# Performance work log

Measured on AMD Instinct MI355X. Metric: run time of the kernel, lower is better.

Reference implementation:

```python
import jax, jax.numpy as jnp
import numpy as np

N, E, H, ED = 10000, 160000, 512, 16
EPS = 1e-5
EDGE_SCALE = 0.1

def _ln(x, g, b):
    mu = jnp.mean(x, axis=-1, keepdims=True)
    var = jnp.mean(jnp.square(x - mu), axis=-1, keepdims=True)
    return (x - mu) * jax.lax.rsqrt(var + EPS) * g + b

def setup_inputs() -> dict:
    key = jax.random.key(0)
    ks = jax.random.split(key, 16)
    def w(k, i, o):
        return jax.random.normal(k, (i, o), jnp.float32) * (1.0 / np.sqrt(i))
    return {
        "h": jax.random.normal(ks[0], (N, H), jnp.float32),
        "edge_attr": jax.random.normal(ks[1], (E, ED), jnp.float32),
        "msg_w1": w(ks[2], H + ED, H), "msg_b1": jnp.zeros((H,), jnp.float32),
        "msg_w2": w(ks[3], H, H),      "msg_b2": jnp.zeros((H,), jnp.float32),
        "upd_w1": w(ks[4], 2 * H, H),  "upd_b1": jnp.zeros((H,), jnp.float32),
        "upd_w2": w(ks[5], H, H),      "upd_b2": jnp.zeros((H,), jnp.float32),
        "norm_g": jnp.ones((H,), jnp.float32), "norm_b": jnp.zeros((H,), jnp.float32),
        "em_w1": w(ks[6], 2 * H + ED, ED), "em_b1": jnp.zeros((ED,), jnp.float32),
        "em_w2": w(ks[7], ED, ED),         "em_b2": jnp.zeros((ED,), jnp.float32),
        "eg_w": w(ks[8], 2 * H + ED, 1),   "eg_b": jnp.zeros((1,), jnp.float32),
        "en_g": jnp.ones((ED,), jnp.float32), "en_b": jnp.zeros((ED,), jnp.float32),
        "edge_index": jax.random.randint(ks[9], (2, E), 0, N, jnp.int32),
    }

def reference(h, edge_attr, msg_w1, msg_b1, msg_w2, msg_b2,
              upd_w1, upd_b1, upd_w2, upd_b2, norm_g, norm_b,
              em_w1, em_b1, em_w2, em_b2, eg_w, eg_b, en_g, en_b,
              edge_index):
    src, dst = edge_index[0], edge_index[1]
    hs = h[src]                      # (E, H)
    hd = h[dst]                      # (E, H)
    # edge update with gating + scaled residual (eval: keep mask == 1)
    z = jnp.concatenate([hs, hd, edge_attr], axis=-1)   # (E, 2H+ED)
    gate = jax.nn.sigmoid(z @ eg_w + eg_b)               # (E, 1)
    delta = jax.nn.gelu(z @ em_w1 + em_b1, approximate=False) @ em_w2 + em_b2
    e_new = _ln(edge_attr + EDGE_SCALE * gate * delta, en_g, en_b)
    # message computation + scatter-add aggregation
    zm = jnp.concatenate([hs, e_new], axis=-1)           # (E, H+ED)
    m = jax.nn.gelu(zm @ msg_w1 + msg_b1, approximate=False) @ msg_w2 + msg_b2
    agg = jax.ops.segment_sum(m, dst, num_segments=h.shape[0])  # (N, H)
    # node update + residual + LayerNorm
    zu = jnp.concatenate([h, agg], axis=-1)              # (N, 2H)
    h2 = jax.nn.gelu(zu @ upd_w1 + upd_b1, approximate=False) @ upd_w2 + upd_b2
    h_out = _ln(h + h2, norm_g, norm_b)
    return (h_out, e_new)
```

## Files before the change

kernel.cpp:

```cpp
#include <hip/hip_runtime.h>

#define N_NODES 10000
#define N_EDGES 160000
#define HD 512
#define EDD 16

typedef unsigned short u16;
typedef __attribute__((ext_vector_type(8))) short bf16x8;
typedef __attribute__((ext_vector_type(4))) float f32x4;
typedef unsigned int u32;

__device__ __forceinline__ float bf2f(u16 u){
  unsigned int x = ((unsigned int)u) << 16;
  return __builtin_bit_cast(float, x);
}
__device__ __forceinline__ u16 f2bf(float f){
  unsigned int x = __builtin_bit_cast(unsigned int, f);
  unsigned int r = (x + 0x7fffu + ((x >> 16) & 1u)) >> 16;
  return (u16)r;
}
__device__ __forceinline__ float ldx(const void* p, long long i, int f32){
  return f32 ? ((const float*)p)[i] : bf2f(((const u16*)p)[i]);
}
__device__ __forceinline__ void stx(void* p, long long i, int f32, float v){
  if (f32) ((float*)p)[i] = v; else ((u16*)p)[i] = f2bf(v);
}
__device__ __forceinline__ float gelu_f(float x){
  float c = x * x;
  float a = x * (1.5957691216f + 0.0713548162f * c);
  float e = __expf(-a);
  return x * __builtin_amdgcn_rcpf(1.0f + e);
}
__device__ __forceinline__ f32x4 mfma16(bf16x8 a, bf16x8 b, f32x4 c){
  return __builtin_amdgcn_mfma_f32_16x16x32_bf16(a, b, c, 0, 0, 0);
}
__device__ __forceinline__ int swz8(int row, int slot){
  return (slot ^ ((row >> 1) & 3)) * 8;
}
__device__ __forceinline__ bf16x8 ld8(const void* p, long long i, int f32){
  if (!f32) return *(const bf16x8*)((const u16*)p + i);
  const float* q = (const float*)p + i;
  float4 a = *(const float4*)q, b = *(const float4*)(q + 4);
  u16 t[8] = { f2bf(a.x), f2bf(a.y), f2bf(a.z), f2bf(a.w),
               f2bf(b.x), f2bf(b.y), f2bf(b.z), f2bf(b.w) };
  return *(const bf16x8*)t;
}
__device__ __forceinline__ void stage8(const void* src, long long idx, int f32, u16* dst){
  bf16x8 v = ld8(src, idx, f32);
  *(bf16x8*)dst = v;
}

__device__ __forceinline__ int probe_rand(const void* p, int l){
  const u16* q = (const u16*)p;
  float mx = 0.f;
  #pragma unroll
  for (int i = 0; i < 4; ++i) mx = fmaxf(mx, fabsf(bf2f(q[l * 4 + i])));
  #pragma unroll
  for (int m = 1; m < 64; m <<= 1) mx = fmaxf(mx, __shfl_xor(mx, m, 64));
  return (mx > 1e3f) ? 1 : 0;
}
__global__ __launch_bounds__(64) void kprobe(
    const void* h, const void* ea, const void* mw1, const void* mw2,
    const void* uw1, const void* uw2, const void* ew1, const void* ew2,
    const void* egw, const void* ng, const void* eng, int* F)
{
  const int l = threadIdx.x;
  int f0 = probe_rand(h, l),   f1 = probe_rand(ea, l),  f2 = probe_rand(mw1, l);
  int f3 = probe_rand(mw2, l), f4 = probe_rand(uw1, l), f5 = probe_rand(uw2, l);
  int f6 = probe_rand(ew1, l), f7 = probe_rand(ew2, l), f8 = probe_rand(egw, l);
  if (l == 0){
    F[0] = f0; F[1] = f1; F[2] = f2; F[3] = f3; F[4] = f4; F[5] = f5;
    F[6] = f6; F[7] = f7; F[8] = f8;
    F[9]  = (((const u16*)ng)[0]  == 0) ? 1 : 0;
    F[10] = (((const u16*)eng)[0] == 0) ? 1 : 0;
    F[11] = f0;
  }
}

__global__ void kfill(u16* __restrict__ out, long long n, float val){
  long long i = (long long)blockIdx.x * 256 + threadIdx.x;
  if (i < n) out[i] = f2bf(val);
}

__global__ __launch_bounds__(256) void kprep(
    const void* __restrict__ h, const void* __restrict__ mw1,
    const void* __restrict__ ew1, const void* __restrict__ egw,
    const void* __restrict__ mb2, const void* __restrict__ uw1,
    const int* __restrict__ F,
    u16* __restrict__ hB, u16* __restrict__ W1T, u16* __restrict__ WceT,
    float* __restrict__ bfused)
{
  __shared__ float tl[64][65];
  const int b = blockIdx.x, tid = threadIdx.x;
  if (b < 2500){
    const long long i = ((long long)b * 256 + tid) * 8;
    if (i < (long long)N_NODES * HD)
      *(bf16x8*)(hB + i) = ld8(h, i, F[0]);
  } else if (b < 2572){
    const int b2 = b - 2500;
    const int kt0 = (b2 >> 3) * 64, nt0 = (b2 & 7) * 64;
    const int ty = tid >> 6, tx = tid & 63;
    const int fw = F[2];
    #pragma unroll
    for (int q = 0; q < 16; ++q){
      const int r = ty * 16 + q;
      const int sr = kt0 + r;
      tl[r][tx] = (sr < 528) ? ldx(mw1, (long long)sr * 512 + nt0 + tx, fw) : 0.f;
    }
    __syncthreads();
    #pragma unroll
    for (int q = 0; q < 16; ++q){
      const int r = ty * 16 + q;
      const int k = kt0 + tx;
      if (k < 544) W1T[(size_t)(nt0 + r) * 544 + k] = f2bf(tl[tx][r]);
    }
  } else if (b < 2668){
    const int i = (b - 2572) * 256 + tid;
    const int c = i >> 9, k = i & 511;
    float v = 0.f;
    if (c < 16)       v = ldx(ew1, (long long)k * 16 + c, F[6]);
    else if (c < 32)  v = ldx(ew1, (long long)(512 + k) * 16 + (c - 16), F[6]);
    else if (c == 32) v = ldx(egw, k, F[8]);
    else if (c == 33) v = ldx(egw, 512 + k, F[8]);
    WceT[i] = f2bf(v);
  } else {
    float* ls   = &tl[0][0];
    float* part = &tl[0][0] + 1024;
    const int f3 = F[3], f4 = F[4];
    for (int j = tid; j < 512; j += 256) ls[j] = ldx(mb2, j, f3);
    __syncthreads();
    const int nn = tid & 31, jg = tid >> 5;
    const int n = (b - 2668) * 32 + nn;
    float a = 0.f;
    for (int jj = 0; jj < 64; ++jj){
      const int j = jg * 64 + jj;
      a += ls[j] * ldx(uw1, (long long)(512 + j) * 512 + n, f4);
    }
    part[jg * 33 + nn] = a;
    __syncthreads();
    if (jg == 0){
      float s = a;
      #pragma unroll
      for (int g = 1; g < 8; ++g) s += part[g * 33 + nn];
      bfused[n] = s;
    }
  }
}

__global__ __launch_bounds__(256) void kprep2(
    const void* __restrict__ uw1, const void* __restrict__ uw2,
    const int* __restrict__ F, u16* __restrict__ WU1T, u16* __restrict__ WU2T)
{
  __shared__ float tl[64][65];
  const int b = blockIdx.x, tid = threadIdx.x;
  const int ty = tid >> 6, tx = tid & 63;
  if (b < 128){
    const int kt0 = (b >> 3) * 64, nt0 = (b & 7) * 64;
    const int fw = F[4];
    #pragma unroll
    for (int q = 0; q < 16; ++q){
      const int r = ty * 16 + q;
      tl[r][tx] = ldx(uw1, (long long)(kt0 + r) * 512 + nt0 + tx, fw);
    }
    __syncthreads();
    #pragma unroll
    for (int q = 0; q < 16; ++q){
      const int r = ty * 16 + q;
      WU1T[(size_t)(nt0 + r) * 1024 + kt0 + tx] = f2bf(tl[tx][r]);
    }
  } else {
    const int b2 = b - 128;
    const int kt0 = (b2 >> 3) * 64, nt0 = (b2 & 7) * 64;
    const int fw = F[5];
    #pragma unroll
    for (int q = 0; q < 16; ++q){
      const int r = ty * 16 + q;
      tl[r][tx] = ldx(uw2, (long long)(kt0 + r) * 512 + nt0 + tx, fw);
    }
    __syncthreads();
    #pragma unroll
    for (int q = 0; q < 16; ++q){
      const int r = ty * 16 + q;
      WU2T[(size_t)(nt0 + r) * 512 + kt0 + tx] = f2bf(tl[tx][r]);
    }
  }
}

__global__ void kdeg(const int* __restrict__ dst, int* __restrict__ deg){
  int e = blockIdx.x * 256 + threadIdx.x;
  if (e < N_EDGES) atomicAdd(&deg[dst[e]], 1);
}

__global__ __launch_bounds__(256) void kscan(const int* __restrict__ deg,
                                             int* __restrict__ start){
  __shared__ int ls[256];
  const int t = threadIdx.x;
  const int base = t * 40;
  int s = 0;
  for (int i = 0; i < 40; ++i){ int idx = base + i; if (idx < N_NODES) s += deg[idx]; }
  ls[t] = s; __syncthreads();
  for (int off = 1; off < 256; off <<= 1){
    int v = (t >= off) ? ls[t - off] : 0;
    __syncthreads();
    ls[t] += v;
    __syncthreads();
  }
  int run = (t == 0) ? 0 : ls[t - 1];
  for (int i = 0; i < 40; ++i){
    int idx = base + i;
    if (idx < N_NODES){ start[idx] = run; run += deg[idx]; }
  }
}

__global__ void kscatter(const int* __restrict__ srcI, const int* __restrict__ dstI,
                         const int* __restrict__ start, int* __restrict__ cursor,
                         int* __restrict__ sSrc, int* __restrict__ sDst,
                         int* __restrict__ sIdx){
  int e = blockIdx.x * 256 + threadIdx.x;
  if (e < N_EDGES){
    int d = dstI[e];
    int p = start[d] + atomicAdd(&cursor[d], 1);
    sSrc[p] = srcI[e]; sDst[p] = d; sIdx[p] = e;
  }
}

__global__ __launch_bounds__(256, 4) void kprePE(
    const u16* __restrict__ hB, const u16* __restrict__ W1T,
    const void* __restrict__ msg_b1, const u16* __restrict__ WceT,
    const int* __restrict__ F, u16* __restrict__ P, u16* __restrict__ PE)
{
  __shared__ u16 As[128 * 32];
  __shared__ u16 Bs[64 * 32];
  const int tid = threadIdx.x;
  const int row0 = blockIdx.x * 128;
  const int w = tid >> 6, l = tid & 63;
  const int lm = l & 15, lk = l >> 4;
  if (blockIdx.y < 8){
    const int fw = F[2];
    const int n0 = blockIdx.y * 64;
    f32x4 acc[2][4];
    f32x4 z4 = {0.f, 0.f, 0.f, 0.f};
    #pragma unroll
    for (int i = 0; i < 2; ++i)
      #pragma unroll
      for (int j = 0; j < 4; ++j) acc[i][j] = z4;
    const int nB = tid >> 2, kqB = tid & 3;
    for (int kt = 0; kt < 16; ++kt){
      const int kk = kt * 32;
      #pragma unroll
      for (int i = 0; i < 2; ++i){
        int t = tid + i * 256;
        int m = t >> 2, kq = t & 3;
        int gr = row0 + m; if (gr > N_NODES - 1) gr = N_NODES - 1;
        *(uint4*)&As[m * 32 + swz8(m, kq)] = *(const uint4*)(hB + (size_t)gr * HD + kk + kq * 8);
      }
      *(uint4*)&Bs[nB * 32 + swz8(nB, kqB)] =
          *(const uint4*)(W1T + (size_t)(n0 + nB) * 544 + kk + kqB * 8);
      __syncthreads();
      bf16x8 af[2], bfv[4];
      #pragma unroll
      for (int i = 0; i < 2; ++i){
        const int R = w * 32 + i * 16 + lm;
        af[i] = *(const bf16x8*)&As[R * 32 + swz8(R, lk)];
      }
      #pragma unroll
      for (int j = 0; j < 4; ++j){
        const int R = j * 16 + lm;
        bfv[j] = *(const bf16x8*)&Bs[R * 32 + swz8(R, lk)];
      }
      #pragma unroll
      for (int i = 0; i < 2; ++i)
        #pragma unroll
        for (int j = 0; j < 4; ++j)
          acc[i][j] = mfma16(af[i], bfv[j], acc[i][j]);
      __syncthreads();
    }
    #pragma unroll
    for (int j = 0; j < 4; ++j){
      const int col = n0 + j * 16 + lm;
      const float bias = ldx(msg_b1, col, fw);
      #pragma unroll
      for (int i = 0; i < 2; ++i){
        const int rb = row0 + w * 32 + i * 16 + lk * 4;
        #pragma unroll
        for (int r = 0; r < 4; ++r){
          int gr = rb + r;
          if (gr < N_NODES)
            P[(size_t)gr * HD + col] = f2bf(acc[i][j][r] + bias);
        }
      }
    }
  } else {
    f32x4 acc[2][3];
    f32x4 z4 = {0.f, 0.f, 0.f, 0.f};
    #pragma unroll
    for (int i = 0; i < 2; ++i)
      #pragma unroll
      for (int j = 0; j < 3; ++j) acc[i][j] = z4;
    for (int kt = 0; kt < 16; ++kt){
      const int kk = kt * 32;
      #pragma unroll
      for (int i = 0; i < 2; ++i){
        int t = tid + i * 256;
        int m = t >> 2, kq = t & 3;
        int gr = row0 + m; if (gr > N_NODES - 1) gr = N_NODES - 1;
        *(uint4*)&As[m * 32 + swz8(m, kq)] = *(const uint4*)(hB + (size_t)gr * HD + kk + kq * 8);
      }
      if (tid < 192){
        int c = tid >> 2, kq = tid & 3;
        *(uint4*)&Bs[c * 32 + swz8(c, kq)] =
            *(const uint4*)(WceT + (size_t)c * 512 + kk + kq * 8);
      }
      __syncthreads();
      bf16x8 af[2], bfv[3];
      #pragma unroll
      for (int i = 0; i < 2; ++i){
        const int R = w * 32 + i * 16 + lm;
        af[i] = *(const bf16x8*)&As[R * 32 + swz8(R, lk)];
      }
      #pragma unroll
      for (int j = 0; j < 3; ++j){
        const int R = j * 16 + lm;
        bfv[j] = *(const bf16x8*)&Bs[R * 32 + swz8(R, lk)];
      }
      #pragma unroll
      for (int i = 0; i < 2; ++i)
        #pragma unroll
        for (int j = 0; j < 3; ++j)
          acc[i][j] = mfma16(af[i], bfv[j], acc[i][j]);
      __syncthreads();
    }
    #pragma unroll
    for (int j = 0; j < 3; ++j){
      const int col = j * 16 + lm;
      #pragma unroll
      for (int i = 0; i < 2; ++i){
        const int rb = row0 + w * 32 + i * 16 + lk * 4;
        #pragma unroll
        for (int r = 0; r < 4; ++r){
          int gr = rb + r;
          if (gr < N_NODES)
            PE[(size_t)gr * 48 + col] = f2bf(acc[i][j][r]);
        }
      }
    }
  }
}

__global__ __launch_bounds__(256) void kedge2(
    const void* __restrict__ ea, const u16* __restrict__ PE,
    const void* __restrict__ em_w1, const void* __restrict__ em_w2,
    const void* __restrict__ em_b1, const void* __restrict__ em_b2,
    const void* __restrict__ eg_w, const void* __restrict__ eg_b,
    const void* __restrict__ en_g, const void* __restrict__ en_b,
    const int* __restrict__ F,
    const int* __restrict__ srcI, const int* __restrict__ dstI,
    void* __restrict__ dout)
{
  __shared__ float wt[16][17];
  __shared__ float w2s[256];
  __shared__ float egt[16], b1e[16], b2s[16], gns[16], bns[16];
  __shared__ float egb_s;
  const int tid = threadIdx.x;
  const int fea = F[1], fem1 = F[6], fem2 = F[7], feg = F[8];
  const int fen = F[10], fo = F[11];
  { int k = tid >> 4, j = tid & 15;
    wt[k][j] = ldx(em_w1, (long long)(1024 + k) * 16 + j, fem1); }
  w2s[tid] = ldx(em_w2, tid, fem2);
  if (tid < 16){
    egt[tid] = ldx(eg_w, 1024 + tid, feg);
    b1e[tid] = ldx(em_b1, tid, fem1);
    b2s[tid] = ldx(em_b2, tid, fem2);
    gns[tid] = ldx(en_g, tid, fen);
    bns[tid] = ldx(en_b, tid, fen);
  }
  if (tid == 0) egb_s = ldx(eg_b, 0, feg);
  __syncthreads();

  const int e = blockIdx.x * 256 + tid;
  const int s = srcI[e], d = dstI[e];
  float earr[16];
  if (fea){
    const float4* q = (const float4*)((const float*)ea + (size_t)e * 16);
    float4 v0 = q[0], v1 = q[1], v2 = q[2], v3 = q[3];
    earr[0]=v0.x; earr[1]=v0.y; earr[2]=v0.z; earr[3]=v0.w;
    earr[4]=v1.x; earr[5]=v1.y; earr[6]=v1.z; earr[7]=v1.w;
    earr[8]=v2.x; earr[9]=v2.y; earr[10]=v2.z; earr[11]=v2.w;
    earr[12]=v3.x; earr[13]=v3.y; earr[14]=v3.z; earr[15]=v3.w;
  } else {
    const u16* q = (const u16*)ea + (size_t)e * 16;
    bf16x8 a = *(const bf16x8*)q, b = *(const bf16x8*)(q + 8);
    #pragma unroll
    for (int j = 0; j < 8; ++j){ earr[j] = bf2f((u16)a[j]); earr[8 + j] = bf2f((u16)b[j]); }
  }
  const u16* prs = PE + (size_t)s * 48;
  const u16* prd = PE + (size_t)d * 48;
  bf16x8 ps0 = *(const bf16x8*)prs,        ps1 = *(const bf16x8*)(prs + 8);
  bf16x8 pd0 = *(const bf16x8*)(prd + 16), pd1 = *(const bf16x8*)(prd + 24);
  const float gs = bf2f(prs[32]), gd = bf2f(prd[33]);
  float t[16];
  #pragma unroll
  for (int j = 0; j < 8; ++j){
    t[j]     = bf2f((u16)ps0[j]) + bf2f((u16)pd0[j]) + b1e[j];
    t[8 + j] = bf2f((u16)ps1[j]) + bf2f((u16)pd1[j]) + b1e[8 + j];
  }
  float gl = gs + gd + egb_s;
  #pragma unroll
  for (int k = 0; k < 16; ++k){
    const float ek = earr[k];
    gl += ek * egt[k];
    #pragma unroll
    for (int j = 0; j < 16; ++j) t[j] += ek * wt[k][j];
  }
  const float gate = __builtin_amdgcn_rcpf(1.0f + __expf(-gl));
  float gj[16];
  #pragma unroll
  for (int j = 0; j < 16; ++j) gj[j] = gelu_f(t[j]);
  float rv[16]; float s1 = 0.f, s2 = 0.f;
  #pragma unroll
  for (int j = 0; j < 16; ++j){
    float dlt = b2s[j];
    #pragma unroll
    for (int k = 0; k < 16; ++k) dlt += gj[k] * w2s[k * 16 + j];
    rv[j] = earr[j] + 0.1f * gate * dlt;
    s1 += rv[j]; s2 += rv[j] * rv[j];
  }
  const float mu  = s1 * (1.f / 16.f);
  const float var = s2 * (1.f / 16.f) - mu * mu;
  const float inv = rsqrtf(var + 1e-5f);
  if (fo){
    float* ob = (float*)dout + (size_t)N_NODES * HD + (size_t)e * 16;
    #pragma unroll
    for (int j = 0; j < 16; ++j) ob[j] = (rv[j] - mu) * inv * gns[j] + bns[j];
  } else {
    u16 tmp[16];
    #pragma unroll
    for (int j = 0; j < 16; ++j) tmp[j] = f2bf((rv[j] - mu) * inv * gns[j] + bns[j]);
    u16* ob = (u16*)dout + (size_t)N_NODES * HD + (size_t)e * 16;
    *(uint4*)ob = *(uint4*)&tmp[0];
    *(uint4*)(ob + 8) = *(uint4*)&tmp[8];
  }
}

__global__ __launch_bounds__(256, 4) void kWf(
    const u16* __restrict__ WU1T, const void* __restrict__ mw2,
    const int* __restrict__ F, u16* __restrict__ WfT)
{
  __shared__ u16 As[128 * 32];
  __shared__ u16 Bs[64 * 32];
  const int tid = threadIdx.x;
  const int f3 = F[3];
  const int row0 = blockIdx.x * 128, n0 = blockIdx.y * 64;
  f32x4 acc[2][4];
  f32x4 z4 = {0.f, 0.f, 0.f, 0.f};
  #pragma unroll
  for (int i = 0; i < 2; ++i)
    #pragma unroll
    for (int j = 0; j < 4; ++j) acc[i][j] = z4;
  const int w = tid >> 6, l = tid & 63;
  const int lm = l & 15, lk = l >> 4;
  const int nB = tid >> 2, kqB = tid & 3;
  for (int kt = 0; kt < 16; ++kt){
    const int kk = kt * 32;
    #pragma unroll
    for (int i = 0; i < 2; ++i){
      int t = tid + i * 256;
      int m = t >> 2, kq = t & 3;
      *(uint4*)&As[m * 32 + swz8(m, kq)] =
          *(const uint4*)(WU1T + (size_t)(row0 + m) * 1024 + 512 + kk + kq * 8);
    }
    stage8(mw2, (long long)(n0 + nB) * 512 + kk + kqB * 8, f3,
           &Bs[nB * 32 + swz8(nB, kqB)]);
    __syncthreads();
    bf16x8 af[2], bfv[4];
    #pragma unroll
    for (int i = 0; i < 2; ++i){
      const int R = w * 32 + i * 16 + lm;
      af[i] = *(const bf16x8*)&As[R * 32 + swz8(R, lk)];
    }
    #pragma unroll
    for (int j = 0; j < 4; ++j){
      const int R = j * 16 + lm;
      bfv[j] = *(const bf16x8*)&Bs[R * 32 + swz8(R, lk)];
    }
    #pragma unroll
    for (int i = 0; i < 2; ++i)
      #pragma unroll
      for (int j = 0; j < 4; ++j)
        acc[i][j] = mfma16(af[i], bfv[j], acc[i][j]);
    __syncthreads();
  }
  #pragma unroll
  for (int j = 0; j < 4; ++j){
    const int col = n0 + j * 16 + lm;
    #pragma unroll
    for (int i = 0; i < 2; ++i){
      const int rb = row0 + w * 32 + i * 16 + lk * 4;
      #pragma unroll
      for (int r = 0; r < 4; ++r)
        WfT[(size_t)(rb + r) * 512 + col] = f2bf(acc[i][j][r]);
    }
  }
}

__global__ __launch_bounds__(256, 4) void kmsg4(
    const u16* __restrict__ P, const void* __restrict__ dout,
    const u16* __restrict__ W1T, const int* __restrict__ F,
    const int* __restrict__ sSrc, const int* __restrict__ sDst,
    const int* __restrict__ sIdx,
    float* __restrict__ agg)
{
  __shared__ __align__(16) float SMEM[4352];
  u16*   As = (u16*)SMEM;
  u16*   Bs = (u16*)SMEM + 4096;
  float* Sf = SMEM;
  __shared__ int src_s[128];
  __shared__ int dst_s[128];
  const int tid = threadIdx.x;
  const int fo = F[11];
  const void* e_base = fo ? (const void*)((const float*)dout + (size_t)N_NODES * HD)
                          : (const void*)((const u16*)dout + (size_t)N_NODES * HD);
  const int row0 = blockIdx.x * 128, n0 = blockIdx.y * 128;
  if (tid < 128){
    src_s[tid] = sSrc[row0 + tid];
    dst_s[tid] = sDst[row0 + tid];
  }
  #pragma unroll
  for (int i = 0; i < 2; ++i){
    int t = tid + i * 256;
    int m = t >> 2, kq = t & 3;
    if (kq < 2){
      const long long ie = sIdx[row0 + m];
      stage8(e_base, ie * EDD + kq * 8, fo, &As[m * 32 + swz8(m, kq)]);
      *(uint4*)&Bs[m * 32 + swz8(m, kq)] =
          *(const uint4*)(W1T + (size_t)(n0 + m) * 544 + 512 + kq * 8);
    } else {
      uint4 z = {0,0,0,0};
      *(uint4*)&As[m * 32 + swz8(m, kq)] = z;
      *(uint4*)&Bs[m * 32 + swz8(m, kq)] = z;
    }
  }
  __syncthreads();
  const int w = tid >> 6, l = tid & 63;
  const int wr = w >> 1, wc = w & 1, lm = l & 15, lk = l >> 4;
  f32x4 acc[4][4];
  bf16x8 af[4], bfv[4];
  #pragma unroll
  for (int i = 0; i < 4; ++i){
    const int R = wr * 64 + i * 16 + lm;
    af[i] = *(const bf16x8*)&As[R * 32 + swz8(R, lk)];
  }
  #pragma unroll
  for (int j = 0; j < 4; ++j){
    const int R = wc * 64 + j * 16 + lm;
    bfv[j] = *(const bf16x8*)&Bs[R * 32 + swz8(R, lk)];
  }
  f32x4 z4 = {0.f, 0.f, 0.f, 0.f};
  #pragma unroll
  for (int i = 0; i < 4; ++i)
    #pragma unroll
    for (int j = 0; j < 4; ++j)
      acc[i][j] = mfma16(af[i], bfv[j], z4);
  u32 poff[4][4];
  #pragma unroll
  for (int i = 0; i < 4; ++i)
    #pragma unroll
    for (int r = 0; r < 4; ++r)
      poff[i][r] = (u32)src_s[wr * 64 + i * 16 + lk * 4 + r] * HD;
  const int cj = tid & 31, chunk = tid >> 5;
  const int rbase = chunk * 16;
  u32 aoff[16]; unsigned maskb = 0;
  {
    int dprev = dst_s[rbase];
    aoff[0] = (u32)dprev * HD;
    #pragma unroll
    for (int rr = 1; rr < 16; ++rr){
      const int dn = dst_s[rbase + rr];
      if (dn == dprev) maskb |= (1u << rr);
      aoff[rr] = (u32)dn * HD;
      dprev = dn;
    }
  }
  __syncthreads();
  const int sfb = wc * 16 + lm;
  #pragma unroll
  for (int j = 0; j < 4; ++j){
    const int col = n0 + wc * 64 + j * 16 + lm;
    #pragma unroll
    for (int i = 0; i < 4; ++i){
      #pragma unroll
      for (int r = 0; r < 4; ++r){
        const int row = wr * 64 + i * 16 + lk * 4 + r;
        const float pv = bf2f(P[poff[i][r] + col]);
        Sf[row * 34 + sfb] = gelu_f(acc[i][j][r] + pv);
      }
    }
    __syncthreads();
    const int acol = n0 + (cj >> 4) * 64 + j * 16 + (cj & 15);
    float run = Sf[rbase * 34 + cj];
    #pragma unroll
    for (int rr = 1; rr < 16; ++rr){
      const float v = Sf[(rbase + rr) * 34 + cj];
      if (maskb & (1u << rr)) run += v;
      else { atomicAdd(&agg[(size_t)aoff[rr - 1] + acol], run); run = v; }
    }
    atomicAdd(&agg[(size_t)aoff[15] + acol], run);
    __syncthreads();
  }
}

__global__ __launch_bounds__(256, 4) void kupd1f(
    const u16* __restrict__ hB, const float* __restrict__ S,
    const u16* __restrict__ WU1T, const u16* __restrict__ WfT,
    const void* __restrict__ upd_b1, const float* __restrict__ bfused,
    const int* __restrict__ deg, const int* __restrict__ F,
    u16* __restrict__ U)
{
  __shared__ u16 As[128 * 32];
  __shared__ u16 Bs[64 * 32];
  const int tid = threadIdx.x;
  const int fw = F[4];
  const int row0 = blockIdx.x * 128, n0 = blockIdx.y * 64;
  f32x4 acc[2][4];
  f32x4 z4 = {0.f, 0.f, 0.f, 0.f};
  #pragma unroll
  for (int i = 0; i < 2; ++i)
    #pragma unroll
    for (int j = 0; j < 4; ++j) acc[i][j] = z4;
  const int w = tid >> 6, l = tid & 63;
  const int lm = l & 15, lk = l >> 4;
  const int nB = tid >> 2, kqB = tid & 3;
  const int am = tid >> 1, ah = tid & 1;
  const int agr = row0 + am;
  for (int kt = 0; kt < 32; ++kt){
    const int kk = kt * 32;
    if (kk < 512){
      #pragma unroll
      for (int i = 0; i < 2; ++i){
        int t = tid + i * 256;
        int m = t >> 2, kq = t & 3;
        int gr = row0 + m; if (gr > N_NODES - 1) gr = N_NODES - 1;
        *(uint4*)&As[m * 32 + swz8(m, kq)] = *(const uint4*)(hB + (size_t)gr * HD + kk + kq * 8);
      }
      *(uint4*)&Bs[nB * 32 + swz8(nB, kqB)] =
          *(const uint4*)(WU1T + (size_t)(n0 + nB) * 1024 + kk + kqB * 8);
    } else {
      const int ks = kk - 512;
      u16 tmp[16];
      if (agr < N_NODES){
        const float4* sp = (const float4*)(S + (size_t)agr * HD + ks + ah * 16);
        #pragma unroll
        for (int q = 0; q < 4; ++q){
          float4 v = sp[q];
          tmp[q*4+0] = f2bf(v.x); tmp[q*4+1] = f2bf(v.y);
          tmp[q*4+2] = f2bf(v.z); tmp[q*4+3] = f2bf(v.w);
        }
      } else {
        #pragma unroll
        for (int q = 0; q < 16; ++q) tmp[q] = 0;
      }
      *(uint4*)&As[am * 32 + swz8(am, ah * 2)]     = *(uint4*)&tmp[0];
      *(uint4*)&As[am * 32 + swz8(am, ah * 2 + 1)] = *(uint4*)&tmp[8];
      *(uint4*)&Bs[nB * 32 + swz8(nB, kqB)] =
          *(const uint4*)(WfT + (size_t)(n0 + nB) * 512 + ks + kqB * 8);
    }
    __syncthreads();
    bf16x8 af[2], bfv[4];
    #pragma unroll
    for (int i = 0; i < 2; ++i){
      const int R = w * 32 + i * 16 + lm;
      af[i] = *(const bf16x8*)&As[R * 32 + swz8(R, lk)];
    }
    #pragma unroll
    for (int j = 0; j < 4; ++j){
      const int R = j * 16 + lm;
      bfv[j] = *(const bf16x8*)&Bs[R * 32 + swz8(R, lk)];
    }
    #pragma unroll
    for (int i = 0; i < 2; ++i)
      #pragma unroll
      for (int j = 0; j < 4; ++j)
        acc[i][j] = mfma16(af[i], bfv[j], acc[i][j]);
    __syncthreads();
  }
  #pragma unroll
  for (int j = 0; j < 4; ++j){
    const int col = n0 + j * 16 + lm;
    const float bias = ldx(upd_b1, col, fw);
    const float bfv2 = bfused[col];
    #pragma unroll
    for (int i = 0; i < 2; ++i){
      const int rb = row0 + w * 32 + i * 16 + lk * 4;
      #pragma unroll
      for (int r = 0; r < 4; ++r){
        int gr = rb + r;
        if (gr < N_NODES)
          U[(size_t)gr * HD + col] =
              f2bf(gelu_f(acc[i][j][r] + bias + (float)deg[gr] * bfv2));
      }
    }
  }
}

__global__ __launch_bounds__(256, 4) void kupd2(
    const u16* __restrict__ U, const u16* __restrict__ WU2T,
    const void* __restrict__ upd_b2, const int* __restrict__ F,
    u16* __restrict__ h2b)
{
  __shared__ u16 As[128 * 32];
  __shared__ u16 Bs[64 * 32];
  const int tid = threadIdx.x;
  const int fw = F[5];
  const int row0 = blockIdx.x * 128, n0 = blockIdx.y * 64;
  f32x4 acc[2][4];
  f32x4 z4 = {0.f, 0.f, 0.f, 0.f};
  #pragma unroll
  for (int i = 0; i < 2; ++i)
    #pragma unroll
    for (int j = 0; j < 4; ++j) acc[i][j] = z4;
  const int w = tid >> 6, l = tid & 63;
  const int lm = l & 15, lk = l >> 4;
  const int nB = tid >> 2, kqB = tid & 3;
  for (int kt = 0; kt < 16; ++kt){
    const int kk = kt * 32;
    #pragma unroll
    for (int i = 0; i < 2; ++i){
      int t = tid + i * 256;
      int m = t >> 2, kq = t & 3;
      int gr = row0 + m; if (gr > N_NODES - 1) gr = N_NODES - 1;
      *(uint4*)&As[m * 32 + swz8(m, kq)] = *(const uint4*)(U + (size_t)gr * HD + kk + kq * 8);
    }
    *(uint4*)&Bs[nB * 32 + swz8(nB, kqB)] =
        *(const uint4*)(WU2T + (size_t)(n0 + nB) * 512 + kk + kqB * 8);
    __syncthreads();
    bf16x8 af[2], bfv[4];
    #pragma unroll
    for (int i = 0; i < 2; ++i){
      const int R = w * 32 + i * 16 + lm;
      af[i] = *(const bf16x8*)&As[R * 32 + swz8(R, lk)];
    }
    #pragma unroll
    for (int j = 0; j < 4; ++j){
      const int R = j * 16 + lm;
      bfv[j] = *(const bf16x8*)&Bs[R * 32 + swz8(R, lk)];
    }
    #pragma unroll
    for (int i = 0; i < 2; ++i)
      #pragma unroll
      for (int j = 0; j < 4; ++j)
        acc[i][j] = mfma16(af[i], bfv[j], acc[i][j]);
    __syncthreads();
  }
  #pragma unroll
  for (int j = 0; j < 4; ++j){
    const int col = n0 + j * 16 + lm;
    const float bias = ldx(upd_b2, col, fw);
    #pragma unroll
    for (int i = 0; i < 2; ++i){
      const int rb = row0 + w * 32 + i * 16 + lk * 4;
      #pragma unroll
      for (int r = 0; r < 4; ++r){
        int gr = rb + r;
        if (gr < N_NODES)
          h2b[(size_t)gr * HD + col] = f2bf(acc[i][j][r] + bias);
      }
    }
  }
}

__global__ __launch_bounds__(256) void kln(
    const void* __restrict__ h, const u16* __restrict__ h2b,
    const void* __restrict__ gg, const void* __restrict__ bbv,
    const int* __restrict__ F, void* __restrict__ dout)
{
  const int fh = F[0], fng = F[9], fo = F[11];
  const int w = threadIdx.x >> 6, l = threadIdx.x & 63;
  const int row = blockIdx.x * 4 + w;
  float x[8];
  #pragma unroll
  for (int j = 0; j < 8; ++j){
    const long long idx = (long long)row * HD + l * 8 + j;
    x[j] = ldx(h, idx, fh) + bf2f(h2b[idx]);
  }
  float s1 = 0.f, s2 = 0.f;
  #pragma unroll
  for (int j = 0; j < 8; ++j){ s1 += x[j]; s2 += x[j] * x[j]; }
  #pragma unroll
  for (int m = 1; m < 64; m <<= 1){ s1 += __shfl_xor(s1, m, 64); s2 += __shfl_xor(s2, m, 64); }
  const float mu  = s1 * (1.f / 512.f);
  const float var = s2 * (1.f / 512.f) - mu * mu;
  const float inv = rsqrtf(var + 1e-5f);
  #pragma unroll
  for (int j = 0; j < 8; ++j){
    const float gf = ldx(gg,  l * 8 + j, fng);
    const float bf = ldx(bbv, l * 8 + j, fng);
    stx(dout, (long long)row * HD + l * 8 + j, fo, (x[j] - mu) * inv * gf + bf);
  }
}

#define OFF_S     0u
#define OFF_DEG   20480000u
#define OFF_CUR   20520000u
#define OFF_F     20560000u
#define OFF_START 20560064u
#define OFF_AGGM  20600064u
#define OFF_W1T   30840064u
#define OFF_W2T   31397120u
#define OFF_WU1T  31921408u
#define OFF_WU2T  32969984u
#define OFF_WET   33494272u
#define OFF_SSRC  33528064u
#define OFF_SDST  34168064u
#define OFF_SIDX  34808064u
#define WS_NEEDED 35448064u

extern "C" void kernel_launch(void* const* d_in, const int* in_sizes, int n_in,
                              void* d_out, int out_size, void* d_ws, size_t ws_size,
                              hipStream_t stream)
{
  const void* h      = d_in[0];
  const void* ea     = d_in[1];
  const void* msg_w1 = d_in[2];
  const void* msg_b1 = d_in[3];
  const void* msg_w2 = d_in[4];
  const void* msg_b2 = d_in[5];
  const void* upd_w1 = d_in[6];
  const void* upd_b1 = d_in[7];
  const void* upd_w2 = d_in[8];
  const void* upd_b2 = d_in[9];
  const void* norm_g = d_in[10];
  const void* norm_b = d_in[11];
  const void* em_w1  = d_in[12];
  const void* em_b1  = d_in[13];
  const void* em_w2  = d_in[14];
  const void* em_b2  = d_in[15];
  const void* eg_w   = d_in[16];
  const void* eg_b   = d_in[17];
  const void* en_g   = d_in[18];
  const void* en_b   = d_in[19];
  const int* eidx    = (const int*)d_in[20];
  const int* srcI = eidx;
  const int* dstI = eidx + N_EDGES;

  float sent = 0.f;
  if (ws_size < (size_t)WS_NEEDED)            sent = 1000.f;
  else if (n_in != 21)                        sent = 2000.f;
  else if (in_sizes[0]  != N_NODES * HD)      sent = 3000.f;
  else if (in_sizes[20] != 2 * N_EDGES)       sent = 4000.f;
  else if (out_size != N_NODES*HD + N_EDGES*EDD) sent = 5000.f;
  if (sent != 0.f){
    kfill<<<(out_size + 255)/256, 256, 0, stream>>>((u16*)d_out, out_size, sent);
    return;
  }

  char* ws = (char*)d_ws;
  float* S      = (float*)(ws + OFF_S);
  u16*   h2b    = (u16*)(ws + OFF_S);
  int*   deg    = (int*)(ws + OFF_DEG);
  int*   cur    = (int*)(ws + OFF_CUR);
  int*   F      = (int*)(ws + OFF_F);
  int*   start  = (int*)(ws + OFF_START);
  u16*   P      = (u16*)(ws + OFF_AGGM);
  u16*   U      = (u16*)(ws + OFF_AGGM);
  u16*   W1T    = (u16*)(ws + OFF_W1T);
  u16*   WfT    = (u16*)(ws + OFF_W2T);
  u16*   PE     = (u16*)(ws + OFF_WU1T);
  u16*   WU1T   = (u16*)(ws + OFF_WU1T);
  u16*   WceT   = (u16*)(ws + OFF_WU2T);
  u16*   WU2T   = (u16*)(ws + OFF_WU2T);
  float* bfused = (float*)(ws + OFF_WET);
  int*   sSrc   = (int*)(ws + OFF_SSRC);
  int*   sDst   = (int*)(ws + OFF_SDST);
  int*   sIdx   = (int*)(ws + OFF_SIDX);

  u16* hB = (u16*)d_out;

  hipMemsetAsync(S, 0, (size_t)OFF_F, stream);

  kprobe<<<1, 64, 0, stream>>>(h, ea, msg_w1, msg_w2, upd_w1, upd_w2,
                               em_w1, em_w2, eg_w, norm_g, en_g, F);

  kprep<<<2684, 256, 0, stream>>>(h, msg_w1, em_w1, eg_w, msg_b2, upd_w1, F,
                                  hB, W1T, WceT, bfused);

  kprePE<<<dim3(79, 9), 256, 0, stream>>>(hB, W1T, msg_b1, WceT, F, P, PE);

  kdeg<<<(N_EDGES + 255)/256, 256, 0, stream>>>(dstI, deg);
  kscan<<<1, 256, 0, stream>>>(deg, start);
  kscatter<<<(N_EDGES + 255)/256, 256, 0, stream>>>(srcI, dstI, start, cur,
                                                    sSrc, sDst, sIdx);

  kedge2<<<625, 256, 0, stream>>>(ea, PE, em_w1, em_w2, em_b1, em_b2, eg_w, eg_b,
                                  en_g, en_b, F, srcI, dstI, d_out);

  kprep2<<<192, 256, 0, stream>>>(upd_w1, upd_w2, F, WU1T, WU2T);
  kWf<<<dim3(4, 8), 256, 0, stream>>>(WU1T, msg_w2, F, WfT);

  kmsg4<<<dim3(1250, 4), 256, 0, stream>>>(P, d_out, W1T, F,
                                           sSrc, sDst, sIdx, S);
  kupd1f<<<dim3(79, 8), 256, 0, stream>>>(hB, S, WU1T, WfT, upd_b1, bfused,
                                          deg, F, U);
  kupd2<<<dim3(79, 8), 256, 0, stream>>>(U, WU2T, upd_b2, F, h2b);
  kln<<<2500, 256, 0, stream>>>(h, h2b, norm_g, norm_b, F, d_out);
}
```

Measured before the change: 411.3 us.

## Stage gathered P rows in LDS with coalesced loads and swap grid axes

In the message kernel, the per-edge gather of precomputed P rows now happens up front: each thread loads four 16-byte vectors per row segment into a padded LDS tile. This replaces scattered 2-byte global loads inside the GELU epilogue loop. Grid dimensions of the GEMM kernels are also swapped so that column tiles for the same row block run back to back, which should improve L2 reuse of the A operand and the gathered rows. The extra LDS tile of about 33 KB raises shared memory per block and may lower occupancy.

```diff
diff --git a/kernel.cpp b/kernel.cpp
--- a/kernel.cpp
+++ b/kernel.cpp
@@ -232,12 +232,12 @@
   __shared__ u16 As[128 * 32];
   __shared__ u16 Bs[64 * 32];
   const int tid = threadIdx.x;
-  const int row0 = blockIdx.x * 128;
+  const int row0 = blockIdx.y * 128;
   const int w = tid >> 6, l = tid & 63;
   const int lm = l & 15, lk = l >> 4;
-  if (blockIdx.y < 8){
+  if (blockIdx.x < 8){
     const int fw = F[2];
-    const int n0 = blockIdx.y * 64;
+    const int n0 = blockIdx.x * 64;
     f32x4 acc[2][4];
     f32x4 z4 = {0.f, 0.f, 0.f, 0.f};
     #pragma unroll
@@ -450,7 +450,7 @@
   __shared__ u16 Bs[64 * 32];
   const int tid = threadIdx.x;
   const int f3 = F[3];
-  const int row0 = blockIdx.x * 128, n0 = blockIdx.y * 64;
+  const int row0 = blockIdx.y * 128, n0 = blockIdx.x * 64;
   f32x4 acc[2][4];
   f32x4 z4 = {0.f, 0.f, 0.f, 0.f};
   #pragma unroll
@@ -503,7 +503,7 @@
   }
 }
 
-__global__ __launch_bounds__(256, 4) void kmsg4(
+__global__ __launch_bounds__(256, 4) void kmsg5(
     const u16* __restrict__ P, const void* __restrict__ dout,
     const u16* __restrict__ W1T, const int* __restrict__ F,
     const int* __restrict__ sSrc, const int* __restrict__ sDst,
@@ -511,20 +511,17 @@
     float* __restrict__ agg)
 {
   __shared__ __align__(16) float SMEM[4352];
+  __shared__ __align__(16) u16 Pl[128 * 132];
+  __shared__ int dst_s[128];
   u16*   As = (u16*)SMEM;
   u16*   Bs = (u16*)SMEM + 4096;
   float* Sf = SMEM;
-  __shared__ int src_s[128];
-  __shared__ int dst_s[128];
   const int tid = threadIdx.x;
   const int fo = F[11];
   const void* e_base = fo ? (const void*)((const float*)dout + (size_t)N_NODES * HD)
                           : (const void*)((const u16*)dout + (size_t)N_NODES * HD);
-  const int row0 = blockIdx.x * 128, n0 = blockIdx.y * 128;
-  if (tid < 128){
-    src_s[tid] = sSrc[row0 + tid];
-    dst_s[tid] = sDst[row0 + tid];
-  }
+  const int row0 = blockIdx.y * 128, n0 = blockIdx.x * 128;
+  if (tid < 128) dst_s[tid] = sDst[row0 + tid];
   #pragma unroll
   for (int i = 0; i < 2; ++i){
     int t = tid + i * 256;
@@ -540,6 +537,18 @@
       *(uint4*)&Bs[m * 32 + swz8(m, kq)] = z;
     }
   }
+  #pragma unroll
+  for (int i = 0; i < 2; ++i){
+    int t = tid + i * 256;
+    int row = t >> 2, seg = t & 3;
+    const uint4* src = (const uint4*)(P + (size_t)sSrc[row0 + row] * HD + n0 + seg * 32);
+    uint4 v0 = src[0], v1 = src[1], v2 = src[2], v3 = src[3];
+    uint2* d = (uint2*)&Pl[row * 132 + seg * 32];
+    d[0] = make_uint2(v0.x, v0.y); d[1] = make_uint2(v0.z, v0.w);
+    d[2] = make_uint2(v1.x, v1.y); d[3] = make_uint2(v1.z, v1.w);
+    d[4] = make_uint2(v2.x, v2.y); d[5] = make_uint2(v2.z, v2.w);
+    d[6] = make_uint2(v3.x, v3.y); d[7] = make_uint2(v3.z, v3.w);
+  }
   __syncthreads();
   const int w = tid >> 6, l = tid & 63;
   const int wr = w >> 1, wc = w & 1, lm = l & 15, lk = l >> 4;
@@ -561,12 +570,6 @@
     #pragma unroll
     for (int j = 0; j < 4; ++j)
       acc[i][j] = mfma16(af[i], bfv[j], z4);
-  u32 poff[4][4];
-  #pragma unroll
-  for (int i = 0; i < 4; ++i)
-    #pragma unroll
-    for (int r = 0; r < 4; ++r)
-      poff[i][r] = (u32)src_s[wr * 64 + i * 16 + lk * 4 + r] * HD;
   const int cj = tid & 31, chunk = tid >> 5;
   const int rbase = chunk * 16;
   u32 aoff[16]; unsigned maskb = 0;
@@ -583,15 +586,15 @@
   }
   __syncthreads();
   const int sfb = wc * 16 + lm;
+  const int plc = wc * 64 + lm;
   #pragma unroll
   for (int j = 0; j < 4; ++j){
-    const int col = n0 + wc * 64 + j * 16 + lm;
     #pragma unroll
     for (int i = 0; i < 4; ++i){
       #pragma unroll
       for (int r = 0; r < 4; ++r){
         const int row = wr * 64 + i * 16 + lk * 4 + r;
-        const float pv = bf2f(P[poff[i][r] + col]);
+        const float pv = bf2f(Pl[row * 132 + plc + j * 16]);
         Sf[row * 34 + sfb] = gelu_f(acc[i][j][r] + pv);
       }
     }
@@ -620,7 +623,7 @@
   __shared__ u16 Bs[64 * 32];
   const int tid = threadIdx.x;
   const int fw = F[4];
-  const int row0 = blockIdx.x * 128, n0 = blockIdx.y * 64;
+  const int row0 = blockIdx.y * 128, n0 = blockIdx.x * 64;
   f32x4 acc[2][4];
   f32x4 z4 = {0.f, 0.f, 0.f, 0.f};
   #pragma unroll
@@ -711,7 +714,7 @@
   __shared__ u16 Bs[64 * 32];
   const int tid = threadIdx.x;
   const int fw = F[5];
-  const int row0 = blockIdx.x * 128, n0 = blockIdx.y * 64;
+  const int row0 = blockIdx.y * 128, n0 = blockIdx.x * 64;
   f32x4 acc[2][4];
   f32x4 z4 = {0.f, 0.f, 0.f, 0.f};
   #pragma unroll
@@ -883,7 +886,7 @@
   kprep<<<2684, 256, 0, stream>>>(h, msg_w1, em_w1, eg_w, msg_b2, upd_w1, F,
                                   hB, W1T, WceT, bfused);
 
-  kprePE<<<dim3(79, 9), 256, 0, stream>>>(hB, W1T, msg_b1, WceT, F, P, PE);
+  kprePE<<<dim3(9, 79), 256, 0, stream>>>(hB, W1T, msg_b1, WceT, F, P, PE);
 
   kdeg<<<(N_EDGES + 255)/256, 256, 0, stream>>>(dstI, deg);
   kscan<<<1, 256, 0, stream>>>(deg, start);
@@ -894,12 +897,12 @@
                                   en_g, en_b, F, srcI, dstI, d_out);
 
   kprep2<<<192, 256, 0, stream>>>(upd_w1, upd_w2, F, WU1T, WU2T);
-  kWf<<<dim3(4, 8), 256, 0, stream>>>(WU1T, msg_w2, F, WfT);
-
-  kmsg4<<<dim3(1250, 4), 256, 0, stream>>>(P, d_out, W1T, F,
+  kWf<<<dim3(8, 4), 256, 0, stream>>>(WU1T, msg_w2, F, WfT);
+
+  kmsg5<<<dim3(4, 1250), 256, 0, stream>>>(P, d_out, W1T, F,
                                            sSrc, sDst, sIdx, S);
-  kupd1f<<<dim3(79, 8), 256, 0, stream>>>(hB, S, WU1T, WfT, upd_b1, bfused,
+  kupd1f<<<dim3(8, 79), 256, 0, stream>>>(hB, S, WU1T, WfT, upd_b1, bfused,
                                           deg, F, U);
-  kupd2<<<dim3(79, 8), 256, 0, stream>>>(U, WU2T, upd_b2, F, h2b);
+  kupd2<<<dim3(8, 79), 256, 0, stream>>>(U, WU2T, upd_b2, F, h2b);
   kln<<<2500, 256, 0, stream>>>(h, h2b, norm_g, norm_b, F, d_out);
 }
```

After: 418.7 us. Within noise of the previous version (+1.8%).
